# Optimization experiments

Hardware: AMD Instinct MI355X
Metric: run time of the kernel (lower is better)

## Reference

```python
import jax, jax.numpy as jnp
import numpy as np

NUM_CLASSES = 1000
GAMMA = 0.9
N = 131072


def setup_inputs() -> dict:
    key = jax.random.key(0)
    k1, k2, k3 = jax.random.split(key, 3)
    preds = jax.random.normal(k1, (N, NUM_CLASSES), dtype=jnp.float32)
    labels = jax.random.randint(k2, (N,), 0, NUM_CLASSES)
    val_preds = jax.random.normal(k3, (NUM_CLASSES, NUM_CLASSES), dtype=jnp.float32)
    return {"preds": preds, "labels": labels, "val_preds": val_preds}


def reference(preds, labels, val_preds):
    # Equivalent of ValScores.update: per-class mean of preds (label-indexed
    # segment reduction) followed by an EMA update, skipping empty classes.
    C = val_preds.shape[0]
    # sums[c] = sum of preds rows with label c   -> [C, C]
    sums = jax.ops.segment_sum(preds, labels, num_segments=C)
    # counts[c] = number of rows with label c    -> [C]
    counts = jax.ops.segment_sum(jnp.ones((preds.shape[0],), preds.dtype),
                                 labels, num_segments=C)
    has = counts > 0
    means = sums / jnp.where(has, counts, jnp.ones_like(counts))[:, None]
    new_val = jnp.where(has[:, None],
                        (1.0 - GAMMA) * means + GAMMA * val_preds,
                        val_preds)
    return new_val
```

## Files before the change

### kernel.cpp

```cpp
#include <hip/hip_runtime.h>

#define NUM_C 1000
#define COLS4 250
#define GAMMA 0.9f

typedef float v4f __attribute__((ext_vector_type(4)));

__global__ void count_rank_kernel(const int* __restrict__ labels,
                                  int* __restrict__ counts,
                                  int* __restrict__ rank, int n) {
    int i = blockIdx.x * blockDim.x + threadIdx.x;
    if (i < n) {
        int l = labels[i];
        rank[i] = atomicAdd(&counts[l], 1);
    }
}

__global__ void scan_kernel(const int* __restrict__ counts,
                            int* __restrict__ offsets) {
    __shared__ int s[1024];
    int tid = threadIdx.x;
    int v = (tid < NUM_C) ? counts[tid] : 0;
    s[tid] = v;
    __syncthreads();
    for (int d = 1; d < 1024; d <<= 1) {
        int x = (tid >= d) ? s[tid - d] : 0;
        __syncthreads();
        s[tid] += x;
        __syncthreads();
    }
    if (tid < NUM_C) offsets[tid] = s[tid] - v;
}

__global__ void scatter_kernel(const int* __restrict__ labels,
                               const int* __restrict__ offsets,
                               const int* __restrict__ rank,
                               int* __restrict__ rowidx, int n) {
    int i = blockIdx.x * blockDim.x + threadIdx.x;
    if (i < n) {
        rowidx[offsets[labels[i]] + rank[i]] = i;
    }
}

__global__ __launch_bounds__(512) void accum_kernel(
        const float* __restrict__ preds, const float* __restrict__ val,
        const int* __restrict__ counts, const int* __restrict__ offsets,
        const int* __restrict__ rowidx, float* __restrict__ out) {
    const int c    = blockIdx.x;
    const int tid  = threadIdx.x;
    const int half = tid >> 8;
    const int lane = tid & 255;
    const bool active = (lane < COLS4);
    const int col4 = active ? lane : 0;

    const v4f* __restrict__ pv = (const v4f*)preds;
    const v4f* __restrict__ vv = (const v4f*)val;
    v4f* __restrict__ ov = (v4f*)out;
    const size_t crow = (size_t)c * COLS4;

    const int nc  = counts[c];
    const int off = offsets[c];

    if (nc == 0) {
        if (half == 0 && active) ov[crow + col4] = vv[crow + col4];
        return;
    }

    __shared__ int rows_s[512];
    __shared__ v4f red[COLS4];

    v4f acc0 = {0.f, 0.f, 0.f, 0.f};
    v4f acc1 = {0.f, 0.f, 0.f, 0.f};

    for (int base = 0; base < nc; base += 512) {
        int m = min(nc - base, 512);
        if (tid < m) rows_s[tid] = rowidx[off + base + tid];
        __syncthreads();

        int r = half;
        for (; r + 6 < m; r += 8) {
            size_t i0 = (size_t)rows_s[r + 0] * COLS4 + col4;
            size_t i1 = (size_t)rows_s[r + 2] * COLS4 + col4;
            size_t i2 = (size_t)rows_s[r + 4] * COLS4 + col4;
            size_t i3 = (size_t)rows_s[r + 6] * COLS4 + col4;
            v4f v0 = pv[i0];
            v4f v1 = pv[i1];
            v4f v2 = pv[i2];
            v4f v3 = pv[i3];
            acc0 += v0 + v1;
            acc1 += v2 + v3;
        }
        for (; r < m; r += 2) {
            size_t i0 = (size_t)rows_s[r] * COLS4 + col4;
            acc0 += pv[i0];
        }
        __syncthreads();
    }

    v4f acc = acc0 + acc1;
    if (half == 1 && active) red[col4] = acc;
    __syncthreads();
    if (half == 0 && active) {
        float inv = 1.0f / (float)nc;
        v4f s = acc + red[col4];
        v4f vp = vv[crow + col4];
        v4f o = (1.0f - GAMMA) * (s * inv) + GAMMA * vp;
        ov[crow + col4] = o;
    }
}

extern "C" void kernel_launch(void* const* d_in, const int* in_sizes, int n_in,
                              void* d_out, int out_size, void* d_ws, size_t ws_size,
                              hipStream_t stream) {
    const float* preds  = (const float*)d_in[0];
    const int*   labels = (const int*)d_in[1];
    const float* val    = (const float*)d_in[2];
    float*       out    = (float*)d_out;
    const int n = in_sizes[1];

    char* ws = (char*)d_ws;
    int* counts  = (int*)(ws + 0);
    int* offsets = (int*)(ws + 4096);
    int* rank    = (int*)(ws + 8192);
    int* rowidx  = (int*)(ws + 8192 + (size_t)n * 4);

    (void)hipMemsetAsync(d_ws, 0, 4096, stream);
    count_rank_kernel<<<(n + 255) / 256, 256, 0, stream>>>(labels, counts, rank, n);
    scan_kernel<<<1, 1024, 0, stream>>>(counts, offsets);
    scatter_kernel<<<(n + 255) / 256, 256, 0, stream>>>(labels, offsets, rank, rowidx, n);
    accum_kernel<<<NUM_C, 512, 0, stream>>>(preds, val, counts, offsets, rowidx, out);
}
```

Baseline: 710.9 us.

## Fuse bucketing into accumulation kernel via per-block label scan

Replaces the memset, count/rank, scan and scatter kernels with one kernel in which each class block scans all labels itself and collects its matching row indices into shared memory through a shared atomic counter. This removes four launches and the global rowidx and rank traffic. In exchange, every block reads the full label array (1000 redundant reads of 512KB, mostly served from L2), and the shared-atomic row order is nondeterministic, so float sums can differ slightly between runs. A fallback path that scans labels directly handles classes with more than 8192 rows.

```diff
diff --git a/kernel.cpp b/kernel.cpp
--- a/kernel.cpp
+++ b/kernel.cpp
@@ -3,49 +3,13 @@
 #define NUM_C 1000
 #define COLS4 250
 #define GAMMA 0.9f
+#define CAP   8192
 
 typedef float v4f __attribute__((ext_vector_type(4)));
 
-__global__ void count_rank_kernel(const int* __restrict__ labels,
-                                  int* __restrict__ counts,
-                                  int* __restrict__ rank, int n) {
-    int i = blockIdx.x * blockDim.x + threadIdx.x;
-    if (i < n) {
-        int l = labels[i];
-        rank[i] = atomicAdd(&counts[l], 1);
-    }
-}
-
-__global__ void scan_kernel(const int* __restrict__ counts,
-                            int* __restrict__ offsets) {
-    __shared__ int s[1024];
-    int tid = threadIdx.x;
-    int v = (tid < NUM_C) ? counts[tid] : 0;
-    s[tid] = v;
-    __syncthreads();
-    for (int d = 1; d < 1024; d <<= 1) {
-        int x = (tid >= d) ? s[tid - d] : 0;
-        __syncthreads();
-        s[tid] += x;
-        __syncthreads();
-    }
-    if (tid < NUM_C) offsets[tid] = s[tid] - v;
-}
-
-__global__ void scatter_kernel(const int* __restrict__ labels,
-                               const int* __restrict__ offsets,
-                               const int* __restrict__ rank,
-                               int* __restrict__ rowidx, int n) {
-    int i = blockIdx.x * blockDim.x + threadIdx.x;
-    if (i < n) {
-        rowidx[offsets[labels[i]] + rank[i]] = i;
-    }
-}
-
-__global__ __launch_bounds__(512) void accum_kernel(
-        const float* __restrict__ preds, const float* __restrict__ val,
-        const int* __restrict__ counts, const int* __restrict__ offsets,
-        const int* __restrict__ rowidx, float* __restrict__ out) {
+__global__ __launch_bounds__(512) void fused_kernel(
+        const float* __restrict__ preds, const int* __restrict__ labels,
+        const float* __restrict__ val, float* __restrict__ out, int n) {
     const int c    = blockIdx.x;
     const int tid  = threadIdx.x;
     const int half = tid >> 8;
@@ -53,32 +17,47 @@
     const bool active = (lane < COLS4);
     const int col4 = active ? lane : 0;
 
+    __shared__ int cnt;
+    __shared__ int rows_s[CAP];
+    __shared__ v4f red[COLS4];
+
+    if (tid == 0) cnt = 0;
+    __syncthreads();
+
+    {
+        const int n4 = n >> 2;
+        const int4* __restrict__ lab4 = (const int4*)labels;
+        for (int i = tid; i < n4; i += 512) {
+            int4 L = lab4[i];
+            int b = i << 2;
+            if (L.x == c) { int p = atomicAdd(&cnt, 1); if (p < CAP) rows_s[p] = b + 0; }
+            if (L.y == c) { int p = atomicAdd(&cnt, 1); if (p < CAP) rows_s[p] = b + 1; }
+            if (L.z == c) { int p = atomicAdd(&cnt, 1); if (p < CAP) rows_s[p] = b + 2; }
+            if (L.w == c) { int p = atomicAdd(&cnt, 1); if (p < CAP) rows_s[p] = b + 3; }
+        }
+        for (int i = (n & ~3) + tid; i < n; i += 512) {
+            if (labels[i] == c) { int p = atomicAdd(&cnt, 1); if (p < CAP) rows_s[p] = i; }
+        }
+    }
+    __syncthreads();
+    const int nc = cnt;
+
     const v4f* __restrict__ pv = (const v4f*)preds;
     const v4f* __restrict__ vv = (const v4f*)val;
     v4f* __restrict__ ov = (v4f*)out;
     const size_t crow = (size_t)c * COLS4;
-
-    const int nc  = counts[c];
-    const int off = offsets[c];
 
     if (nc == 0) {
         if (half == 0 && active) ov[crow + col4] = vv[crow + col4];
         return;
     }
 
-    __shared__ int rows_s[512];
-    __shared__ v4f red[COLS4];
-
     v4f acc0 = {0.f, 0.f, 0.f, 0.f};
     v4f acc1 = {0.f, 0.f, 0.f, 0.f};
 
-    for (int base = 0; base < nc; base += 512) {
-        int m = min(nc - base, 512);
-        if (tid < m) rows_s[tid] = rowidx[off + base + tid];
-        __syncthreads();
-
+    if (nc <= CAP) {
         int r = half;
-        for (; r + 6 < m; r += 8) {
+        for (; r + 6 < nc; r += 8) {
             size_t i0 = (size_t)rows_s[r + 0] * COLS4 + col4;
             size_t i1 = (size_t)rows_s[r + 2] * COLS4 + col4;
             size_t i2 = (size_t)rows_s[r + 4] * COLS4 + col4;
@@ -90,11 +69,13 @@
             acc0 += v0 + v1;
             acc1 += v2 + v3;
         }
-        for (; r < m; r += 2) {
-            size_t i0 = (size_t)rows_s[r] * COLS4 + col4;
-            acc0 += pv[i0];
+        for (; r < nc; r += 2) {
+            acc0 += pv[(size_t)rows_s[r] * COLS4 + col4];
         }
-        __syncthreads();
+    } else {
+        for (int i = half; i < n; i += 2) {
+            if (labels[i] == c) acc0 += pv[(size_t)i * COLS4 + col4];
+        }
     }
 
     v4f acc = acc0 + acc1;
@@ -118,15 +99,5 @@
     float*       out    = (float*)d_out;
     const int n = in_sizes[1];
 
-    char* ws = (char*)d_ws;
-    int* counts  = (int*)(ws + 0);
-    int* offsets = (int*)(ws + 4096);
-    int* rank    = (int*)(ws + 8192);
-    int* rowidx  = (int*)(ws + 8192 + (size_t)n * 4);
-
-    (void)hipMemsetAsync(d_ws, 0, 4096, stream);
-    count_rank_kernel<<<(n + 255) / 256, 256, 0, stream>>>(labels, counts, rank, n);
-    scan_kernel<<<1, 1024, 0, stream>>>(counts, offsets);
-    scatter_kernel<<<(n + 255) / 256, 256, 0, stream>>>(labels, offsets, rank, rowidx, n);
-    accum_kernel<<<NUM_C, 512, 0, stream>>>(preds, val, counts, offsets, rowidx, out);
+    fused_kernel<<<NUM_C, 512, 0, stream>>>(preds, labels, val, out, n);
 }
```

Result: no change. 703.6 us (-1.0%).
